# Optimization experiments

Measured on AMD Instinct MI355X. Metric: run time of the kernel, lower is better.

## Reference

```python
import jax, jax.numpy as jnp
import numpy as np

TOPK = 32  # init kwarg topk=32, method='softmax'


def setup_inputs() -> dict:
    key = jax.random.key(0)
    k1, k2 = jax.random.split(key)
    X1 = jax.random.normal(k1, (8192, 64), dtype=jnp.float32)
    X2 = jax.random.normal(k2, (8192, 64), dtype=jnp.float32)
    return {"X1": X1, "X2": X2}


def reference(X1, X2):
    # pairwise Euclidean distance via the matmul expansion (same math as torch.cdist p=2)
    sq = (
        jnp.sum(X1 * X1, axis=-1)[:, None]
        + jnp.sum(X2 * X2, axis=-1)[None, :]
        - 2.0 * (X1 @ X2.T)
    )  # [N1, N2]
    neg_dist = -jnp.sqrt(jnp.maximum(sq, 0.0))
    # top-k along dim=1, softmax over the k selected values
    val, idx = jax.lax.top_k(neg_dist, TOPK)          # [N1, K]
    score = jax.nn.softmax(val, axis=1)               # [N1, K]
    # scatter scores back into a dense zero matrix
    rows = jnp.arange(neg_dist.shape[0])[:, None]     # [N1, 1]
    out = jnp.zeros_like(neg_dist).at[rows, idx].set(score)
    return out, score
```

## Files before the change

### kernel.cpp

```cpp
#include <hip/hip_runtime.h>
#include <math.h>
#include <float.h>
#include <limits.h>

#define N 8192
#define D 64
#define TOPK 32
#define TILE 128
#define CAP 1024
#define CAP2 256
#define MARGIN 1.0f

typedef _Float16 f16x8 __attribute__((ext_vector_type(8)));
typedef _Float16 f16x4v __attribute__((ext_vector_type(4)));
typedef __attribute__((ext_vector_type(4))) float f32x4;

__device__ __forceinline__ unsigned ford(float f) {
    unsigned u = __float_as_uint(f);
    return u ^ ((u & 0x80000000u) ? 0xFFFFFFFFu : 0x80000000u);
}
__device__ __forceinline__ float finv(unsigned u) {
    unsigned b = (u & 0x80000000u) ? (u ^ 0x80000000u) : ~u;
    return __uint_as_float(b);
}

__global__ __launch_bounds__(256) void prep_kernel(
    const float* __restrict__ X1, const float* __restrict__ X2,
    float* __restrict__ nrm,
    _Float16* __restrict__ X1f, _Float16* __restrict__ X2f)
{
    int id = blockIdx.x * blockDim.x + threadIdx.x;
    if (id >= 2 * N) return;
    const float* X = (id < N) ? X1 : X2;
    _Float16* H = (id < N) ? X1f : X2f;
    int r = (id < N) ? id : id - N;
    const float4* p = (const float4*)(X + (size_t)r * D);
    f16x4v* ph = (f16x4v*)(H + (size_t)r * D);
    float s = 0.f;
#pragma unroll
    for (int q = 0; q < D / 4; ++q) {
        float4 v = p[q];
        s += v.x * v.x + v.y * v.y + v.z * v.z + v.w * v.w;
        f16x4v h;
        h[0] = (_Float16)v.x; h[1] = (_Float16)v.y;
        h[2] = (_Float16)v.z; h[3] = (_Float16)v.w;
        ph[q] = h;
    }
    nrm[id] = s;
}

#define MFMA16F(a, b, c) __builtin_amdgcn_mfma_f32_16x16x32_f16((a), (b), (c), 0, 0, 0)

__device__ __forceinline__ void stage_tile(
    const _Float16* __restrict__ gsrc, _Float16* __restrict__ lds, int t)
{
    const f16x8* g = (const f16x8*)gsrc;
#pragma unroll
    for (int it = 0; it < 4; ++it) {
        int idx = it * 256 + t;
        int row = idx >> 3;
        int co  = (idx & 7) << 3;
        int sw  = co ^ ((row & 7) << 3);
        *(f16x8*)&lds[row * 64 + sw] = g[idx];
    }
}

__device__ __forceinline__ void mfma_core_lds(
    const _Float16* __restrict__ Asm, const _Float16* __restrict__ Bsm,
    int wr, int wc, int lane, f32x4 acc[4][4])
{
    const int l15 = lane & 15;
    const int lg8 = (lane >> 4) * 8;

    f16x8 ah[4][2];
#pragma unroll
    for (int mt = 0; mt < 4; ++mt) {
        int row = wr * 64 + mt * 16 + l15;
        int sw0 = (lg8)      ^ ((row & 7) << 3);
        int sw1 = (32 + lg8) ^ ((row & 7) << 3);
        ah[mt][0] = *(const f16x8*)&Asm[row * 64 + sw0];
        ah[mt][1] = *(const f16x8*)&Asm[row * 64 + sw1];
    }
#pragma unroll
    for (int nt = 0; nt < 4; ++nt) {
        int row = wc * 64 + nt * 16 + l15;
        int sw0 = (lg8)      ^ ((row & 7) << 3);
        int sw1 = (32 + lg8) ^ ((row & 7) << 3);
        f16x8 b0 = *(const f16x8*)&Bsm[row * 64 + sw0];
        f16x8 b1 = *(const f16x8*)&Bsm[row * 64 + sw1];
#pragma unroll
        for (int mt = 0; mt < 4; ++mt) {
            acc[mt][nt] = MFMA16F(ah[mt][0], b0, acc[mt][nt]);
            acc[mt][nt] = MFMA16F(ah[mt][1], b1, acc[mt][nt]);
        }
    }
}

__global__ __launch_bounds__(256) void mfma_s_kernel(
    const _Float16* __restrict__ X1f, const _Float16* __restrict__ X2f,
    const float* __restrict__ nrm, _Float16* __restrict__ S,
    float* __restrict__ tmax)
{
    __shared__ _Float16 smem[TILE * TILE];
    __shared__ float red[128][2];

    _Float16* Asm = smem;
    _Float16* Bsm = smem + TILE * D;

    const int t = threadIdx.x;
    const int lane = t & 63, w = t >> 6;
    const int wr = w >> 1, wc = w & 1;
    const int row0 = blockIdx.y * TILE, col0 = blockIdx.x * TILE;
    const int l15 = lane & 15, lg = lane >> 4;

    stage_tile(X1f + (size_t)row0 * D, Asm, t);
    stage_tile(X2f + (size_t)col0 * D, Bsm, t);
    __syncthreads();

    f32x4 acc[4][4];
#pragma unroll
    for (int mt = 0; mt < 4; ++mt)
#pragma unroll
        for (int nt = 0; nt < 4; ++nt)
            acc[mt][nt] = (f32x4){0.f, 0.f, 0.f, 0.f};

    mfma_core_lds(Asm, Bsm, wr, wc, lane, acc);

    float nb[4];
#pragma unroll
    for (int nt = 0; nt < 4; ++nt) nb[nt] = nrm[N + col0 + wc * 64 + nt * 16 + l15];

    __syncthreads();

    float rmax[4][4];
#pragma unroll
    for (int mt = 0; mt < 4; ++mt) {
#pragma unroll
        for (int reg = 0; reg < 4; ++reg) {
            int lrow = wr * 64 + mt * 16 + lg * 4 + reg;
            float na = nrm[row0 + lrow];
            float rm = -FLT_MAX;
#pragma unroll
            for (int nt = 0; nt < 4; ++nt) {
                float v = -fmaxf(na + nb[nt] - 2.0f * acc[mt][nt][reg], 0.f);
                _Float16 h = (_Float16)v;
                smem[lrow * TILE + wc * 64 + nt * 16 + l15] = h;
                rm = fmaxf(rm, (float)h);
            }
            rmax[mt][reg] = rm;
        }
    }
    __syncthreads();

#pragma unroll
    for (int it = 0; it < 8; ++it) {
        int idx = it * 256 + t;
        int row = idx >> 4;
        int c8  = (idx & 15) << 3;
        *(f16x8*)(S + (size_t)(row0 + row) * N + col0 + c8) =
            *(const f16x8*)&smem[row * TILE + c8];
    }

#pragma unroll
    for (int off = 1; off < 16; off <<= 1)
#pragma unroll
        for (int mt = 0; mt < 4; ++mt)
#pragma unroll
            for (int reg = 0; reg < 4; ++reg)
                rmax[mt][reg] = fmaxf(rmax[mt][reg], __shfl_xor(rmax[mt][reg], off));

    if (l15 == 0) {
#pragma unroll
        for (int mt = 0; mt < 4; ++mt)
#pragma unroll
            for (int reg = 0; reg < 4; ++reg)
                red[wr * 64 + mt * 16 + lg * 4 + reg][wc] = rmax[mt][reg];
    }
    __syncthreads();
    if (t < 128)
        tmax[(size_t)(row0 + t) * 64 + blockIdx.x] = fmaxf(red[t][0], red[t][1]);
}

__global__ __launch_bounds__(256) void thr_kernel(
    const float* __restrict__ tmax, float* __restrict__ thr)
{
    const int t = threadIdx.x;
    const int w = t >> 6;
    const int lane = t & 63;
    const int r = blockIdx.x * 4 + w;

    float tm = tmax[(size_t)r * 64 + lane];
    unsigned km = ford(tm);
    int rk = 0;
#pragma unroll
    for (int l = 0; l < 64; ++l) {
        unsigned o = __shfl(km, l);
        rk += (o > km || (o == km && l < lane)) ? 1 : 0;
    }
    unsigned long long bm = __ballot(rk == 31);
    float tv = __shfl(tm, __ffsll(bm) - 1);
    if (lane == 0) thr[r] = tv - MARGIN;
}

__global__ __launch_bounds__(256) void fused_topk_kernel(
    const float* __restrict__ X1, const float* __restrict__ X2,
    const float* __restrict__ nrm, const float* __restrict__ thr,
    const _Float16* __restrict__ S, float* __restrict__ out,
    float* __restrict__ score_out)
{
    __shared__ float x1r[4][D];
    __shared__ unsigned short lst[4][CAP2];
    __shared__ unsigned long long kl[4][CAP2];
    __shared__ int scnt[4];

    const int t = threadIdx.x;
    const int w = t >> 6;
    const int lane = t & 63;
    const int r = blockIdx.x * 4 + w;

    x1r[w][lane] = X1[(size_t)r * D + lane];
    if (lane == 0) scnt[w] = 0;
    const float th = thr[r];
    __builtin_amdgcn_s_waitcnt(0xC07F);

    const _Float16* Sr = S + (size_t)r * N;
#pragma unroll 4
    for (int c = 0; c < 16; ++c) {
        f16x8 h8 = *(const f16x8*)(Sr + (size_t)(c * 64 + lane) * 8);
#pragma unroll
        for (int q = 0; q < 8; ++q) {
            float v = (float)h8[q];
            if (v >= th) {
                int p = atomicAdd(&scnt[w], 1);
                if (p < CAP2)
                    lst[w][p] = (unsigned short)((c * 64 + lane) * 8 + q);
            }
        }
    }
    __builtin_amdgcn_s_waitcnt(0xC07F);
    const int n = min(scnt[w], CAP2);

    float na = nrm[r];
    for (int q = lane; q < n; q += 64) {
        int col = lst[w][q];
        const float4* xr = (const float4*)(X2 + (size_t)col * D);
        float dot = 0.f;
#pragma unroll
        for (int i = 0; i < D / 4; ++i) {
            float4 xv = xr[i];
            dot += x1r[w][4 * i + 0] * xv.x + x1r[w][4 * i + 1] * xv.y
                 + x1r[w][4 * i + 2] * xv.z + x1r[w][4 * i + 3] * xv.w;
        }
        float v = -fmaxf(na + nrm[N + col] - 2.0f * dot, 0.f);
        kl[w][q] = ((unsigned long long)ford(v) << 32) | (unsigned)(8191 - col);
    }
    __builtin_amdgcn_s_waitcnt(0xC07F);

    unsigned long long mykey = 0ull;
    for (int it = 0; it < TOPK; ++it) {
        unsigned long long b = 0ull; int bp = 0;
        for (int q = lane; q < n; q += 64) {
            unsigned long long kk = kl[w][q];
            if (kk > b) { b = kk; bp = q; }
        }
        for (int off = 32; off > 0; off >>= 1) {
            unsigned long long ob = __shfl_down(b, off);
            int op = __shfl_down(bp, off);
            if (ob > b) { b = ob; bp = op; }
        }
        unsigned long long b0 = __shfl(b, 0);
        int bp0 = __shfl(bp, 0);
        if (lane == it) { mykey = b0; kl[w][bp0] = 0ull; }
    }

    float myv = 0.f; int myj = 0;
    if (lane < TOPK) {
        float sv = finv((unsigned)(mykey >> 32));
        myv = -sqrtf(-sv);
        myj = 8191 - (int)(mykey & 0xFFFFFFFFu);
    }
    float Mx = __shfl(myv, 0);
    float e = (lane < TOPK) ? expf(myv - Mx) : 0.f;
    float Z = e;
    for (int off = 32; off > 0; off >>= 1) Z += __shfl_xor(Z, off);
    float s = e / Z;
    if (lane < TOPK) score_out[(size_t)r * TOPK + lane] = s;

    float* row = out + (size_t)r * N;
    const float4 zz = make_float4(0.f, 0.f, 0.f, 0.f);
#pragma unroll 8
    for (int c = 0; c < 32; ++c) ((float4*)row)[c * 64 + lane] = zz;
    __builtin_amdgcn_s_waitcnt(0x0F70);
    if (lane < TOPK) row[myj] = s;
}

__global__ __launch_bounds__(256) void norms_kernel(
    const float* __restrict__ X1, const float* __restrict__ X2,
    float* __restrict__ nrm)
{
    int id = blockIdx.x * blockDim.x + threadIdx.x;
    if (id >= 2 * N) return;
    const float* X = (id < N) ? X1 : X2;
    int r = (id < N) ? id : id - N;
    const float4* p = (const float4*)(X + (size_t)r * D);
    float s = 0.f;
#pragma unroll
    for (int q = 0; q < D / 4; ++q) {
        float4 v = p[q];
        s += v.x * v.x + v.y * v.y + v.z * v.z + v.w * v.w;
    }
    nrm[id] = s;
}

__global__ __launch_bounds__(256, 2) void dist_kernel(
    const float* __restrict__ X1, const float* __restrict__ X2,
    const float* __restrict__ nrm, float* __restrict__ out,
    float* __restrict__ tmax, int have_tmax)
{
    __shared__ float As[D * TILE];
    __shared__ float Bs[D * TILE];

    const int t = threadIdx.x;
    const int row0 = blockIdx.y * TILE;
    const int col0 = blockIdx.x * TILE;

#pragma unroll
    for (int p = 0; p < 8; ++p) {
        int lin = p * 256 + t;
        int r   = lin >> 4;
        int d4  = (lin & 15) << 2;
        int g   = (d4 >> 2) & 7;
        int cb  = r ^ (g << 3);
        float4 a = *(const float4*)(X1 + (size_t)(row0 + r) * D + d4);
        As[(d4 + 0) * TILE + cb] = a.x;
        As[(d4 + 1) * TILE + cb] = a.y;
        As[(d4 + 2) * TILE + cb] = a.z;
        As[(d4 + 3) * TILE + cb] = a.w;
        float4 b = *(const float4*)(X2 + (size_t)(col0 + r) * D + d4);
        Bs[(d4 + 0) * TILE + cb] = b.x;
        Bs[(d4 + 1) * TILE + cb] = b.y;
        Bs[(d4 + 2) * TILE + cb] = b.z;
        Bs[(d4 + 3) * TILE + cb] = b.w;
    }
    __syncthreads();

    const int tx = t & 15;
    const int ty = t >> 4;
    float acc[8][8] = {};

#pragma unroll 8
    for (int k = 0; k < D; ++k) {
        int gk  = (k >> 2) & 7;
        int ab  = k * TILE + ((ty ^ gk) << 3);
        int bb0 = k * TILE + ((4 * tx) ^ (gk << 3));
        float4 a0 = *(const float4*)&As[ab];
        float4 a1 = *(const float4*)&As[ab + 4];
        float4 b0 = *(const float4*)&Bs[bb0];
        float4 b1 = *(const float4*)&Bs[bb0 + 64];
        float av[8] = {a0.x, a0.y, a0.z, a0.w, a1.x, a1.y, a1.z, a1.w};
        float bv[8] = {b0.x, b0.y, b0.z, b0.w, b1.x, b1.y, b1.z, b1.w};
#pragma unroll
        for (int i = 0; i < 8; ++i)
#pragma unroll
            for (int j = 0; j < 8; ++j)
                acc[i][j] += av[i] * bv[j];
    }

    float na[8], nb[8];
#pragma unroll
    for (int i = 0; i < 8; ++i) na[i] = nrm[row0 + 8 * ty + i];
#pragma unroll
    for (int q = 0; q < 4; ++q) {
        nb[q]     = nrm[N + col0 + 4 * tx + q];
        nb[4 + q] = nrm[N + col0 + 64 + 4 * tx + q];
    }

    float rmax[8];
#pragma unroll
    for (int i = 0; i < 8; ++i) rmax[i] = -FLT_MAX;

#pragma unroll
    for (int i = 0; i < 8; ++i) {
        float* po = out + (size_t)(row0 + 8 * ty + i) * N + col0 + 4 * tx;
        float4 o0, o1;
        float* f0 = (float*)&o0;
        float* f1 = (float*)&o1;
#pragma unroll
        for (int q = 0; q < 4; ++q) {
            float s0 = na[i] + nb[q] - 2.0f * acc[i][q];
            f0[q] = -fmaxf(s0, 0.0f);
            float s1 = na[i] + nb[4 + q] - 2.0f * acc[i][4 + q];
            f1[q] = -fmaxf(s1, 0.0f);
            rmax[i] = fmaxf(rmax[i], fmaxf(f0[q], f1[q]));
        }
        *(float4*)po        = o0;
        *(float4*)(po + 64) = o1;
    }

    if (have_tmax) {
#pragma unroll
        for (int i = 0; i < 8; ++i) {
            float mv = rmax[i];
            mv = fmaxf(mv, __shfl_down(mv, 8, 16));
            mv = fmaxf(mv, __shfl_down(mv, 4, 16));
            mv = fmaxf(mv, __shfl_down(mv, 2, 16));
            mv = fmaxf(mv, __shfl_down(mv, 1, 16));
            if (tx == 0)
                tmax[(size_t)(row0 + 8 * ty + i) * 64 + blockIdx.x] = mv;
        }
    }
}

__global__ __launch_bounds__(256) void topk_kernel(
    float* __restrict__ out, float* __restrict__ score_out,
    const float* __restrict__ tmax, int have_tmax)
{
    __shared__ unsigned long long candl[4][CAP];
    __shared__ int scnt[4];

    const int t    = threadIdx.x;
    const int w    = t >> 6;
    const int lane = t & 63;
    const int r    = blockIdx.x * 4 + w;
    float* row = out + (size_t)r * N;
    const float4* row4 = (const float4*)row;

    float thr;
    float lm = -FLT_MAX;
    if (have_tmax) {
        float tm = tmax[(size_t)r * 64 + lane];
        unsigned km = ford(tm);
        int rk = 0;
#pragma unroll
        for (int l = 0; l < 64; ++l) {
            unsigned o = __shfl(km, l);
            rk += (o > km || (o == km && l < lane)) ? 1 : 0;
        }
        unsigned long long bm = __ballot(rk == 31);
        thr = __shfl(tm, __ffsll(bm) - 1);
    } else {
#pragma unroll 8
        for (int c = 0; c < 32; ++c) {
            float4 x = row4[c * 64 + lane];
            lm = fmaxf(lm, fmaxf(fmaxf(x.x, x.y), fmaxf(x.z, x.w)));
        }
        thr = lm;
        for (int off = 32; off > 0; off >>= 1)
            thr = fminf(thr, __shfl_xor(thr, off));
    }

    for (int attempt = 0; ; ++attempt) {
        if (lane == 0) scnt[w] = 0;
        __builtin_amdgcn_s_waitcnt(0xC07F);
        for (int c = 0; c < 32; ++c) {
            float4 x = row4[c * 64 + lane];
            float vs[4] = {x.x, x.y, x.z, x.w};
#pragma unroll
            for (int q = 0; q < 4; ++q) {
                float v = vs[q];
                lm = fmaxf(lm, v);
                if (v >= thr) {
                    int p = atomicAdd(&scnt[w], 1);
                    if (p < CAP) {
                        unsigned long long key =
                            ((unsigned long long)ford(v) << 32) |
                            (unsigned)(8191 - (4 * (c * 64 + lane) + q));
                        candl[w][p] = key;
                    }
                }
            }
        }
        __builtin_amdgcn_s_waitcnt(0xC07F);
        if (scnt[w] <= CAP || attempt == 1) break;
        unsigned kml = ford(lm);
        int rk2 = 0;
#pragma unroll
        for (int l = 0; l < 64; ++l) {
            unsigned o = __shfl(kml, l);
            rk2 += (o < kml || (o == kml && l < lane)) ? 1 : 0;
        }
        unsigned long long bm2 = __ballot(rk2 == 15);
        float t2 = __shfl(lm, __ffsll(bm2) - 1);
        thr = fmaxf(thr, t2);
    }
    const int n = min(scnt[w], CAP);

    unsigned long long mykey = 0ull;
    for (int it = 0; it < TOPK; ++it) {
        unsigned long long b = 0ull; int bp = 0;
        for (int q = lane; q < n; q += 64) {
            unsigned long long kk = candl[w][q];
            if (kk > b) { b = kk; bp = q; }
        }
        for (int off = 32; off > 0; off >>= 1) {
            unsigned long long ob = __shfl_down(b, off);
            int op = __shfl_down(bp, off);
            if (ob > b) { b = ob; bp = op; }
        }
        unsigned long long b0 = __shfl(b, 0);
        int bp0 = __shfl(bp, 0);
        if (lane == it) { mykey = b0; candl[w][bp0] = 0ull; }
    }

    float myv = 0.f; int myj = 0;
    if (lane < TOPK) {
        float sv = finv((unsigned)(mykey >> 32));
        myv = -sqrtf(-sv);
        myj = 8191 - (int)(mykey & 0xFFFFFFFFu);
    }
    float Mx = __shfl(myv, 0);
    float e = (lane < TOPK) ? expf(myv - Mx) : 0.f;
    float Z = e;
    for (int off = 32; off > 0; off >>= 1) Z += __shfl_xor(Z, off);
    float s = e / Z;
    if (lane < TOPK) score_out[(size_t)r * TOPK + lane] = s;

    const float4 zz = make_float4(0.f, 0.f, 0.f, 0.f);
#pragma unroll 8
    for (int c = 0; c < 32; ++c) ((float4*)row)[c * 64 + lane] = zz;
    __builtin_amdgcn_s_waitcnt(0x0F70);
    if (lane < TOPK) row[myj] = s;
}

extern "C" void kernel_launch(void* const* d_in, const int* in_sizes, int n_in,
                              void* d_out, int out_size, void* d_ws, size_t ws_size,
                              hipStream_t stream)
{
    const float* X1 = (const float*)d_in[0];
    const float* X2 = (const float*)d_in[1];
    float* out = (float*)d_out;
    float* score = out + (size_t)N * N;

    char* base = (char*)d_ws;
    float* nrm  = (float*)base;
    float* tmax = nrm + 2 * N;
    float* thrv = tmax + (size_t)N * 64;
    _Float16* X1f = (_Float16*)(thrv + N);
    _Float16* X2f = X1f + (size_t)N * D;
    _Float16* S   = X2f + (size_t)N * D;

    size_t need_new = (size_t)(2 * N + (size_t)N * 64 + N) * sizeof(float)
                    + 2 * (size_t)N * D * sizeof(_Float16)
                    + (size_t)N * N * sizeof(_Float16);
    size_t need_old = (size_t)(2 * N + (size_t)N * 64) * sizeof(float);

    if (ws_size >= need_new) {
        prep_kernel<<<(2 * N + 255) / 256, 256, 0, stream>>>(X1, X2, nrm, X1f, X2f);
        dim3 grid(N / TILE, N / TILE);
        mfma_s_kernel<<<grid, 256, 0, stream>>>(X1f, X2f, nrm, S, tmax);
        thr_kernel<<<N / 4, 256, 0, stream>>>(tmax, thrv);
        fused_topk_kernel<<<N / 4, 256, 0, stream>>>(
            X1, X2, nrm, thrv, S, out, score);
    } else {
        float* tmax_f = nrm + 2 * N;
        int have_tmax = (ws_size >= need_old) ? 1 : 0;
        norms_kernel<<<(2 * N + 255) / 256, 256, 0, stream>>>(X1, X2, nrm);
        dim3 grid(N / TILE, N / TILE);
        dist_kernel<<<grid, 256, 0, stream>>>(X1, X2, nrm, out, tmax_f, have_tmax);
        topk_kernel<<<N / 4, 256, 0, stream>>>(out, score, tmax_f, have_tmax);
    }
}
```

Measured before the change: 382.7 us.

## Fuse threshold into top-k, skip low-max S chunks, move zero-fill into GEMM

The separate threshold kernel is folded into the top-k kernel, which now computes the 32nd-largest tile max per row itself and keeps the tile maxima in shared memory. During the scan, each 128-column chunk of S is read only when its tile max reaches the threshold, which cuts most of the fp16 S reads. Zeroing of the dense output moves from the top-k kernel into the MFMA kernel, so each block writes its own output tile while its staging loads are in flight. The GEMM kernel now carries the full 256 MB zero-fill write, and the scan has per-lane divergent branches.

```diff
diff --git a/kernel.cpp b/kernel.cpp
--- a/kernel.cpp
+++ b/kernel.cpp
@@ -96,10 +96,10 @@
     }
 }
 
-__global__ __launch_bounds__(256) void mfma_s_kernel(
+__global__ __launch_bounds__(256) void mfma_sz_kernel(
     const _Float16* __restrict__ X1f, const _Float16* __restrict__ X2f,
     const float* __restrict__ nrm, _Float16* __restrict__ S,
-    float* __restrict__ tmax)
+    float* __restrict__ tmax, float* __restrict__ out)
 {
     __shared__ _Float16 smem[TILE * TILE];
     __shared__ float red[128][2];
@@ -115,6 +115,15 @@
 
     stage_tile(X1f + (size_t)row0 * D, Asm, t);
     stage_tile(X2f + (size_t)col0 * D, Bsm, t);
+
+    const float4 zz = make_float4(0.f, 0.f, 0.f, 0.f);
+#pragma unroll
+    for (int p = 0; p < 16; ++p) {
+        int lin = p * 256 + t;
+        int rr = lin >> 5;
+        int c4 = (lin & 31) << 2;
+        *(float4*)(out + (size_t)(row0 + rr) * N + col0 + c4) = zz;
+    }
     __syncthreads();
 
     f32x4 acc[4][4];
@@ -181,15 +190,28 @@
         tmax[(size_t)(row0 + t) * 64 + blockIdx.x] = fmaxf(red[t][0], red[t][1]);
 }
 
-__global__ __launch_bounds__(256) void thr_kernel(
-    const float* __restrict__ tmax, float* __restrict__ thr)
-{
+__global__ __launch_bounds__(256) void fused_topk_kernel(
+    const float* __restrict__ X1, const float* __restrict__ X2,
+    const float* __restrict__ nrm, const float* __restrict__ tmax,
+    const _Float16* __restrict__ S, float* __restrict__ out,
+    float* __restrict__ score_out)
+{
+    __shared__ float x1r[4][D];
+    __shared__ float stm[4][64];
+    __shared__ unsigned short lst[4][CAP2];
+    __shared__ unsigned long long kl[4][CAP2];
+    __shared__ int scnt[4];
+
     const int t = threadIdx.x;
     const int w = t >> 6;
     const int lane = t & 63;
     const int r = blockIdx.x * 4 + w;
 
+    x1r[w][lane] = X1[(size_t)r * D + lane];
     float tm = tmax[(size_t)r * 64 + lane];
+    stm[w][lane] = tm;
+    if (lane == 0) scnt[w] = 0;
+
     unsigned km = ford(tm);
     int rk = 0;
 #pragma unroll
@@ -198,42 +220,23 @@
         rk += (o > km || (o == km && l < lane)) ? 1 : 0;
     }
     unsigned long long bm = __ballot(rk == 31);
-    float tv = __shfl(tm, __ffsll(bm) - 1);
-    if (lane == 0) thr[r] = tv - MARGIN;
-}
-
-__global__ __launch_bounds__(256) void fused_topk_kernel(
-    const float* __restrict__ X1, const float* __restrict__ X2,
-    const float* __restrict__ nrm, const float* __restrict__ thr,
-    const _Float16* __restrict__ S, float* __restrict__ out,
-    float* __restrict__ score_out)
-{
-    __shared__ float x1r[4][D];
-    __shared__ unsigned short lst[4][CAP2];
-    __shared__ unsigned long long kl[4][CAP2];
-    __shared__ int scnt[4];
-
-    const int t = threadIdx.x;
-    const int w = t >> 6;
-    const int lane = t & 63;
-    const int r = blockIdx.x * 4 + w;
-
-    x1r[w][lane] = X1[(size_t)r * D + lane];
-    if (lane == 0) scnt[w] = 0;
-    const float th = thr[r];
+    const float th = __shfl(tm, __ffsll(bm) - 1) - MARGIN;
+
     __builtin_amdgcn_s_waitcnt(0xC07F);
 
     const _Float16* Sr = S + (size_t)r * N;
-#pragma unroll 4
     for (int c = 0; c < 16; ++c) {
-        f16x8 h8 = *(const f16x8*)(Sr + (size_t)(c * 64 + lane) * 8);
-#pragma unroll
-        for (int q = 0; q < 8; ++q) {
-            float v = (float)h8[q];
-            if (v >= th) {
-                int p = atomicAdd(&scnt[w], 1);
-                if (p < CAP2)
-                    lst[w][p] = (unsigned short)((c * 64 + lane) * 8 + q);
+        int st = c * 4 + (lane >> 4);
+        if (stm[w][st] >= th) {
+            f16x8 h8 = *(const f16x8*)(Sr + (size_t)(c * 64 + lane) * 8);
+#pragma unroll
+            for (int q = 0; q < 8; ++q) {
+                float v = (float)h8[q];
+                if (v >= th) {
+                    int p = atomicAdd(&scnt[w], 1);
+                    if (p < CAP2)
+                        lst[w][p] = (unsigned short)((c * 64 + lane) * 8 + q);
+                }
             }
         }
     }
@@ -284,14 +287,10 @@
     float Z = e;
     for (int off = 32; off > 0; off >>= 1) Z += __shfl_xor(Z, off);
     float s = e / Z;
-    if (lane < TOPK) score_out[(size_t)r * TOPK + lane] = s;
-
-    float* row = out + (size_t)r * N;
-    const float4 zz = make_float4(0.f, 0.f, 0.f, 0.f);
-#pragma unroll 8
-    for (int c = 0; c < 32; ++c) ((float4*)row)[c * 64 + lane] = zz;
-    __builtin_amdgcn_s_waitcnt(0x0F70);
-    if (lane < TOPK) row[myj] = s;
+    if (lane < TOPK) {
+        score_out[(size_t)r * TOPK + lane] = s;
+        out[(size_t)r * N + myj] = s;
+    }
 }
 
 __global__ __launch_bounds__(256) void norms_kernel(
@@ -534,12 +533,11 @@
     char* base = (char*)d_ws;
     float* nrm  = (float*)base;
     float* tmax = nrm + 2 * N;
-    float* thrv = tmax + (size_t)N * 64;
-    _Float16* X1f = (_Float16*)(thrv + N);
+    _Float16* X1f = (_Float16*)(tmax + (size_t)N * 64);
     _Float16* X2f = X1f + (size_t)N * D;
     _Float16* S   = X2f + (size_t)N * D;
 
-    size_t need_new = (size_t)(2 * N + (size_t)N * 64 + N) * sizeof(float)
+    size_t need_new = (size_t)(2 * N + (size_t)N * 64) * sizeof(float)
                     + 2 * (size_t)N * D * sizeof(_Float16)
                     + (size_t)N * N * sizeof(_Float16);
     size_t need_old = (size_t)(2 * N + (size_t)N * 64) * sizeof(float);
@@ -547,10 +545,9 @@
     if (ws_size >= need_new) {
         prep_kernel<<<(2 * N + 255) / 256, 256, 0, stream>>>(X1, X2, nrm, X1f, X2f);
         dim3 grid(N / TILE, N / TILE);
-        mfma_s_kernel<<<grid, 256, 0, stream>>>(X1f, X2f, nrm, S, tmax);
-        thr_kernel<<<N / 4, 256, 0, stream>>>(tmax, thrv);
+        mfma_sz_kernel<<<grid, 256, 0, stream>>>(X1f, X2f, nrm, S, tmax, out);
         fused_topk_kernel<<<N / 4, 256, 0, stream>>>(
-            X1, X2, nrm, thrv, S, out, score);
+            X1, X2, nrm, tmax, S, out, score);
     } else {
         float* tmax_f = nrm + 2 * N;
         int have_tmax = (ws_size >= need_old) ? 1 : 0;
```

Result: slower. 443.9 us (+16.0%).
